# Performance work log

Hardware: AMD Instinct MI355X
Metric: run time of the kernel (lower is better)

The kernel has to match this reference:

```python
import jax, jax.numpy as jnp
import numpy as np

DIM = 3456      # visual_dim
E = 1024        # embed_dim = dim_head*heads = 128*8
H = 8
D = E // H
LN_EPS = 1e-5


def _mlp(x, w1, b1, w2, b2):
    # nn.Sequential(Linear, GELU(exact), Linear)
    h = jax.nn.gelu(x @ w1.T + b1, approximate=False)
    return h @ w2.T + b2


def _ln(x, g, b):
    m = jnp.mean(x, axis=-1, keepdims=True)
    v = jnp.mean((x - m) ** 2, axis=-1, keepdims=True)
    return (x - m) * jax.lax.rsqrt(v + LN_EPS) * g + b


def setup_inputs() -> dict:
    key = jax.random.key(0)
    ks = jax.random.split(key, 24)
    std = 0.02
    d = {"x": jax.random.normal(ks[0], (5, 729, DIM), dtype=jnp.float32)}
    i = 1
    for name in ("q", "k", "v"):
        d[f"{name}_w1"] = std * jax.random.normal(ks[i], (E, DIM), dtype=jnp.float32); i += 1
        d[f"{name}_b1"] = jnp.zeros((E,), jnp.float32)
        d[f"{name}_w2"] = std * jax.random.normal(ks[i], (E, E), dtype=jnp.float32); i += 1
        d[f"{name}_b2"] = jnp.zeros((E,), jnp.float32)
        d[f"ln_{name}_g"] = jnp.ones((E,), jnp.float32)
        d[f"ln_{name}_b"] = jnp.zeros((E,), jnp.float32)
    d["in_proj_w"] = std * jax.random.normal(ks[i], (3 * E, E), dtype=jnp.float32); i += 1
    d["in_proj_b"] = jnp.zeros((3 * E,), jnp.float32)
    d["out_proj_w"] = std * jax.random.normal(ks[i], (E, E), dtype=jnp.float32); i += 1
    d["out_proj_b"] = jnp.zeros((E,), jnp.float32)
    d["to_out_w"] = std * jax.random.normal(ks[i], (DIM, E), dtype=jnp.float32)
    return d


def reference(x,
              q_w1, q_b1, q_w2, q_b2, ln_q_g, ln_q_b,
              k_w1, k_b1, k_w2, k_b2, ln_k_g, ln_k_b,
              v_w1, v_b1, v_w2, v_b2, ln_v_g, ln_v_b,
              in_proj_w, in_proj_b, out_proj_w, out_proj_b, to_out_w):
    t, hw, c = x.shape
    # spatial_temporal pattern: x_multi = x, no interpolation.
    # q/k/v: MLP -> LN -> permute(1,0,2) -> divide_feature -> flatten.
    # divide_feature is a pure permutation of tokens; all tokens end up in a
    # single (L, 1, E) attention, so full attention over the flattened
    # (hw, t) token order computes the identical result.
    q = _ln(_mlp(x, q_w1, q_b1, q_w2, q_b2), ln_q_g, ln_q_b)  # (t, hw, E)
    k = _ln(_mlp(x, k_w1, k_b1, k_w2, k_b2), ln_k_g, ln_k_b)
    v = _ln(_mlp(x, v_w1, v_b1, v_w2, v_b2), ln_v_g, ln_v_b)
    L = t * hw
    q = q.transpose(1, 0, 2).reshape(L, E)  # (hw*t, E), (h,w,t)-major order
    k = k.transpose(1, 0, 2).reshape(L, E)
    v = v.transpose(1, 0, 2).reshape(L, E)
    # nn.MultiheadAttention with packed in_proj
    qp = (q @ in_proj_w[:E].T + in_proj_b[:E]).reshape(L, H, D)
    kp = (k @ in_proj_w[E:2 * E].T + in_proj_b[E:2 * E]).reshape(L, H, D)
    vp = (v @ in_proj_w[2 * E:].T + in_proj_b[2 * E:]).reshape(L, H, D)
    scale = 1.0 / jnp.sqrt(jnp.asarray(D, q.dtype))
    scores = jnp.einsum('qhd,khd->hqk', qp, kp) * scale  # (H, L, L)
    attn = jax.nn.softmax(scores, axis=-1)
    o = jnp.einsum('hqk,khd->qhd', attn, vp).reshape(L, E)
    o = o @ out_proj_w.T + out_proj_b
    o = o.reshape(hw, t, E).transpose(1, 0, 2)  # (t, hw, E)
    out = o @ to_out_w.T                         # (t, hw, c)
    return x + out
```

## Files before the change

### kernel.cpp

```cpp
#include <hip/hip_runtime.h>
#include <hip/hip_bf16.h>

#define L_TOK 3645
#define MP    3712
#define DIMV  3456
#define EDIM  1024

typedef __attribute__((ext_vector_type(8))) short bf8;
typedef __attribute__((ext_vector_type(4))) short s4v;
typedef __attribute__((ext_vector_type(4))) float f4;

__device__ __forceinline__ short f2b(float f) {
  union { float f; unsigned u; } v; v.f = f;
  unsigned r = v.u + 0x7fffu + ((v.u >> 16) & 1u);
  return (short)(r >> 16);
}
__device__ __forceinline__ float b2f(short s) {
  union { unsigned u; float f; } v; v.u = ((unsigned)(unsigned short)s) << 16;
  return v.f;
}
__device__ __forceinline__ void gld16(const void* g, void* l) {
  __builtin_amdgcn_global_load_lds(
      (const __attribute__((address_space(1))) void*)(unsigned long long)g,
      (__attribute__((address_space(3))) void*)(unsigned)(unsigned long long)l,
      16, 0, 0);
}

__global__ __launch_bounds__(256) void k_cvt(const float* __restrict__ src,
                                             short* __restrict__ dst, int n4) {
  int i = blockIdx.x * 256 + threadIdx.x;
  if (i >= n4) return;
  float4 v = ((const float4*)src)[i];
  s4v o; o[0] = f2b(v.x); o[1] = f2b(v.y); o[2] = f2b(v.z); o[3] = f2b(v.w);
  ((s4v*)dst)[i] = o;
}
__global__ __launch_bounds__(256) void k_cvt_pad(const float* __restrict__ src,
                                                 short* __restrict__ dst, int n4src, int n4tot) {
  int i = blockIdx.x * 256 + threadIdx.x;
  if (i >= n4tot) return;
  s4v o; o[0] = 0; o[1] = 0; o[2] = 0; o[3] = 0;
  if (i < n4src) {
    float4 v = ((const float4*)src)[i];
    o[0] = f2b(v.x); o[1] = f2b(v.y); o[2] = f2b(v.z); o[3] = f2b(v.w);
  }
  ((s4v*)dst)[i] = o;
}

#define GM_GELU   0
#define GM_BIAS   1
#define GM_QSCALE 2
#define GM_RESID  3

template<int MODE>
__global__ __launch_bounds__(256)
void k_gemm(const short* __restrict__ A, long sA,
            const short* __restrict__ B, long sB,
            const float* __restrict__ bias0, const float* __restrict__ bias1,
            const float* __restrict__ bias2,
            void* __restrict__ Cout, long sC,
            int N, int K, const float* __restrict__ resid)
{
  __shared__ short As[128 * 32];
  __shared__ short Bs[128 * 32];
  const int tid  = threadIdx.x;
  const int z    = blockIdx.z;
  const int brow = blockIdx.y * 128;
  const int bcol = blockIdx.x * 128;
  const short* Ab = A + (long)z * sA;
  const short* Bb = B + (long)z * sB;
  const float* bias = (z == 0) ? bias0 : (z == 1 ? bias1 : bias2);

  const int wave = tid >> 6, lane = tid & 63;
  const int lg = lane >> 4, lc = lane & 15;
  const int m0 = (wave >> 1) * 64, n0 = (wave & 1) * 64;

  const int r0 = tid >> 2, seg = tid & 3;
  const int r1 = r0 + 64;
  const int so0 = (seg ^ ((r0 >> 1) & 3)) * 8;
  const int so1 = (seg ^ ((r1 >> 1) & 3)) * 8;
  const short* gA0 = Ab + (long)(brow + r0) * K + so0;
  const short* gA1 = Ab + (long)(brow + r1) * K + so1;
  const short* gB0 = Bb + (long)(bcol + r0) * K + so0;
  const short* gB1 = Bb + (long)(bcol + r1) * K + so1;
  short* lA0 = &As[tid * 8];
  short* lA1 = &As[(tid + 256) * 8];
  short* lB0 = &Bs[tid * 8];
  short* lB1 = &Bs[(tid + 256) * 8];

  f4 acc[4][4];
  f4 zero = {0.f, 0.f, 0.f, 0.f};
#pragma unroll
  for (int i = 0; i < 4; ++i)
#pragma unroll
    for (int j = 0; j < 4; ++j) acc[i][j] = zero;

  for (int kt = 0; kt < K; kt += 32) {
    gld16(gA0, lA0); gld16(gA1, lA1);
    gld16(gB0, lB0); gld16(gB1, lB1);
    gA0 += 32; gA1 += 32; gB0 += 32; gB1 += 32;
    __syncthreads();
    bf8 af[4], bfr[4];
#pragma unroll
    for (int mi = 0; mi < 4; ++mi) {
      int r = m0 + mi * 16 + lc;
      af[mi] = *(const bf8*)&As[r * 32 + ((lg ^ ((r >> 1) & 3)) * 8)];
    }
#pragma unroll
    for (int ni = 0; ni < 4; ++ni) {
      int r = n0 + ni * 16 + lc;
      bfr[ni] = *(const bf8*)&Bs[r * 32 + ((lg ^ ((r >> 1) & 3)) * 8)];
    }
#pragma unroll
    for (int mi = 0; mi < 4; ++mi)
#pragma unroll
      for (int ni = 0; ni < 4; ++ni)
        acc[mi][ni] = __builtin_amdgcn_mfma_f32_16x16x32_bf16(af[mi], bfr[ni], acc[mi][ni], 0, 0, 0);
    __syncthreads();
  }

  if (MODE == GM_RESID) {
    float* C = (float*)Cout;
#pragma unroll
    for (int ni = 0; ni < 4; ++ni) {
      int col = bcol + n0 + ni * 16 + lc;
#pragma unroll
      for (int mi = 0; mi < 4; ++mi)
#pragma unroll
        for (int r = 0; r < 4; ++r) {
          int row = brow + m0 + mi * 16 + lg * 4 + r;
          if (row < L_TOK)
            C[(long)row * N + col] = acc[mi][ni][r] + resid[(long)row * N + col];
        }
    }
  } else {
    short* C = (short*)Cout + (long)z * sC;
    const float alpha = (MODE == GM_QSCALE && z == 0) ? 0.08838834764831845f : 1.0f;
#pragma unroll
    for (int ni = 0; ni < 4; ++ni) {
      int col = bcol + n0 + ni * 16 + lc;
      float bv = bias[col];
#pragma unroll
      for (int mi = 0; mi < 4; ++mi)
#pragma unroll
        for (int r = 0; r < 4; ++r) {
          int row = brow + m0 + mi * 16 + lg * 4 + r;
          float v = acc[mi][ni][r] + bv;
          if (MODE == GM_GELU) v = 0.5f * v * (1.f + erff(v * 0.70710678118654752f));
          v *= alpha;
          C[(long)row * EDIM + col] = f2b(v);
        }
    }
  }
}

__global__ __launch_bounds__(256)
void k_ln(const short* __restrict__ A, short* __restrict__ Y,
          const float* __restrict__ g0, const float* __restrict__ g1, const float* __restrict__ g2,
          const float* __restrict__ b0, const float* __restrict__ b1, const float* __restrict__ b2)
{
  const int row = blockIdx.x, z = blockIdx.y;
  const float* g = (z == 0) ? g0 : (z == 1 ? g1 : g2);
  const float* b = (z == 0) ? b0 : (z == 1 ? b1 : b2);
  const short* a = A + ((long)z * MP + row) * EDIM;
  short* y = Y + ((long)z * MP + row) * EDIM;
  const int t = threadIdx.x;
  s4v v = *(const s4v*)&a[t * 4];
  float x0 = b2f(v[0]), x1 = b2f(v[1]), x2 = b2f(v[2]), x3 = b2f(v[3]);
  float s = x0 + x1 + x2 + x3;
  float q = x0 * x0 + x1 * x1 + x2 * x2 + x3 * x3;
#pragma unroll
  for (int off = 1; off < 64; off <<= 1) { s += __shfl_xor(s, off); q += __shfl_xor(q, off); }
  __shared__ float rs[4], rq[4];
  if ((t & 63) == 0) { rs[t >> 6] = s; rq[t >> 6] = q; }
  __syncthreads();
  s = rs[0] + rs[1] + rs[2] + rs[3];
  q = rq[0] + rq[1] + rq[2] + rq[3];
  float mean = s * (1.f / 1024.f);
  float var  = q * (1.f / 1024.f) - mean * mean;
  float rstd = rsqrtf(var + 1e-5f);
  s4v o;
#pragma unroll
  for (int j = 0; j < 4; ++j) {
    int col = t * 4 + j;
    o[j] = f2b((b2f(v[j]) - mean) * rstd * g[col] + b[col]);
  }
  *(s4v*)&y[t * 4] = o;
}

__global__ __launch_bounds__(256)
void k_vtrans(const short* __restrict__ vp, short* __restrict__ vpT)
{
  const int kb = blockIdx.x * 64, h = blockIdx.y;
  __shared__ short T[64 * 128];
  const int tid = threadIdx.x;
#pragma unroll
  for (int i = 0; i < 4; ++i) {
    int c = tid + 256 * i;
    int r = c >> 4, x = c & 15;
    bf8 val = *(const bf8*)&vp[(long)(kb + r) * EDIM + h * 128 + x * 8];
    *(bf8*)&T[r * 128 + ((x ^ (r & 7)) * 8)] = val;
  }
  __syncthreads();
#pragma unroll
  for (int i = 0; i < 4; ++i) {
    int c = tid + 256 * i;
    int dr = c >> 3, x = c & 7;
    short tmp[8];
#pragma unroll
    for (int e = 0; e < 8; ++e) {
      int kv = x * 8 + e;
      tmp[e] = T[kv * 128 + (((dr >> 3) ^ (kv & 7)) << 3) + (dr & 7)];
    }
    *(bf8*)&vpT[((long)h * 128 + dr) * MP + kb + x * 8] = *(bf8*)tmp;
  }
}

__global__ __launch_bounds__(256)
void k_attn(const short* __restrict__ qp, const short* __restrict__ kp,
            const short* __restrict__ vpT, short* __restrict__ o)
{
  const int bx = blockIdx.x;
  const int h = bx & 7, qb = (bx >> 3) * 64;
  const int tid = threadIdx.x, wave = tid >> 6, lane = tid & 63;
  const int lg = lane >> 4, lc = lane & 15;
  __shared__ short Ks[64 * 128];
  __shared__ short Vs[128 * 64];
  __shared__ short Ps[4][16 * 64];

  const int qrow = qb + wave * 16 + lc;
  bf8 qf[4];
#pragma unroll
  for (int d4 = 0; d4 < 4; ++d4)
    qf[d4] = *(const bf8*)&qp[(long)qrow * EDIM + h * 128 + d4 * 32 + lg * 8];

  f4 oacc[8];
  f4 zero = {0.f, 0.f, 0.f, 0.f};
#pragma unroll
  for (int dt = 0; dt < 8; ++dt) oacc[dt] = zero;
  float lsum = 0.f;

  for (int kb = 0; kb < L_TOK; kb += 64) {
#pragma unroll
    for (int i = 0; i < 4; ++i) {
      int c = tid + 256 * i; int r = c >> 4, x = c & 15;
      gld16(&kp[(long)(kb + r) * EDIM + h * 128 + (x ^ (r & 7)) * 8], &Ks[c * 8]);
    }
#pragma unroll
    for (int i = 0; i < 4; ++i) {
      int c = tid + 256 * i; int dr = c >> 3, x = c & 7;
      gld16(&vpT[((long)h * 128 + dr) * MP + kb + (x ^ (dr & 7)) * 8], &Vs[c * 8]);
    }
    __syncthreads();

#pragma unroll
    for (int s = 0; s < 4; ++s) {
      f4 sa = zero;
      const int krow = s * 16 + lc;
#pragma unroll
      for (int d4 = 0; d4 < 4; ++d4) {
        bf8 kf = *(const bf8*)&Ks[krow * 128 + (((d4 * 4 + lg) ^ (krow & 7)) * 8)];
        sa = __builtin_amdgcn_mfma_f32_16x16x32_bf16(kf, qf[d4], sa, 0, 0, 0);
      }
      const int kvb = kb + s * 16 + lg * 4;
      float p[4];
#pragma unroll
      for (int r = 0; r < 4; ++r) {
        float e = __expf(sa[r]);
        p[r] = (kvb + r < L_TOK) ? e : 0.f;
        lsum += p[r];
      }
      s4v pk; pk[0] = f2b(p[0]); pk[1] = f2b(p[1]); pk[2] = f2b(p[2]); pk[3] = f2b(p[3]);
      *(s4v*)&Ps[wave][lc * 64 + ((s * 16 + lg * 4) ^ ((lc & 7) << 3))] = pk;
    }
    bf8 pf0 = *(const bf8*)&Ps[wave][lc * 64 + ((lg * 8) ^ ((lc & 7) << 3))];
    bf8 pf1 = *(const bf8*)&Ps[wave][lc * 64 + ((32 + lg * 8) ^ ((lc & 7) << 3))];
#pragma unroll
    for (int dt = 0; dt < 8; ++dt) {
      const int vrow = dt * 16 + lc;
      bf8 vf0 = *(const bf8*)&Vs[vrow * 64 + ((lg ^ (vrow & 7)) * 8)];
      bf8 vf1 = *(const bf8*)&Vs[vrow * 64 + (((4 + lg) ^ (vrow & 7)) * 8)];
      oacc[dt] = __builtin_amdgcn_mfma_f32_16x16x32_bf16(pf0, vf0, oacc[dt], 0, 0, 0);
      oacc[dt] = __builtin_amdgcn_mfma_f32_16x16x32_bf16(pf1, vf1, oacc[dt], 0, 0, 0);
    }
    __syncthreads();
  }

  lsum += __shfl_xor(lsum, 16);
  lsum += __shfl_xor(lsum, 32);
  float rinv[4];
#pragma unroll
  for (int r = 0; r < 4; ++r) rinv[r] = 1.f / __shfl(lsum, lg * 4 + r);
#pragma unroll
  for (int dt = 0; dt < 8; ++dt)
#pragma unroll
    for (int r = 0; r < 4; ++r) {
      int orow = qb + wave * 16 + lg * 4 + r;
      o[(long)orow * EDIM + h * 128 + dt * 16 + lc] = f2b(oacc[dt][r] * rinv[r]);
    }
}

extern "C" void kernel_launch(void* const* d_in, const int* in_sizes, int n_in,
                              void* d_out, int out_size, void* d_ws, size_t ws_size,
                              hipStream_t stream)
{
  const float* x   = (const float*)d_in[0];
  const float* ipb = (const float*)d_in[20];
  const float* opb = (const float*)d_in[22];

  char* ws = (char*)d_ws;
  short* regA = (short*)(ws + 0);
  short* regB = (short*)(ws + 25657344);
  short* w1b  = (short*)(ws + 48463872);
  short* w2b  = (short*)(ws + 69697536);
  short* wpb  = (short*)(ws + 75988992);
  short* wob  = (short*)(ws + 82280448);
  short* wtb  = (short*)(ws + 84377600);
  short* vpT  = (short*)(ws + 91455488);

  short* xb  = regA;
  short* h1  = regB;
  short* aln = regA;
  short* lnq = regB;
  short* proj = regA;
  short* ob  = regB;
  short* o2  = (short*)(ws + 25657344 + 7602176);

  k_cvt_pad<<<12528, 256, 0, stream>>>(x, xb, 3149280, 3207168);
  k_cvt<<<3456, 256, 0, stream>>>((const float*)d_in[1],  w1b,            884736);
  k_cvt<<<3456, 256, 0, stream>>>((const float*)d_in[7],  w1b + 3538944,  884736);
  k_cvt<<<3456, 256, 0, stream>>>((const float*)d_in[13], w1b + 7077888,  884736);
  k_cvt<<<1024, 256, 0, stream>>>((const float*)d_in[3],  w2b,            262144);
  k_cvt<<<1024, 256, 0, stream>>>((const float*)d_in[9],  w2b + 1048576,  262144);
  k_cvt<<<1024, 256, 0, stream>>>((const float*)d_in[15], w2b + 2097152,  262144);
  k_cvt<<<3072, 256, 0, stream>>>((const float*)d_in[19], wpb,            786432);
  k_cvt<<<1024, 256, 0, stream>>>((const float*)d_in[21], wob,            262144);
  k_cvt<<<3456, 256, 0, stream>>>((const float*)d_in[23], wtb,            884736);

  dim3 g3(8, 29, 3), g1(8, 29, 1);
  k_gemm<GM_GELU><<<g3, 256, 0, stream>>>(xb, 0, w1b, 3538944,
      (const float*)d_in[2], (const float*)d_in[8], (const float*)d_in[14],
      h1, (long)MP * EDIM, EDIM, DIMV, nullptr);
  k_gemm<GM_BIAS><<<g3, 256, 0, stream>>>(h1, (long)MP * EDIM, w2b, 1048576,
      (const float*)d_in[4], (const float*)d_in[10], (const float*)d_in[16],
      aln, (long)MP * EDIM, EDIM, EDIM, nullptr);
  dim3 gl(MP, 3);
  k_ln<<<gl, 256, 0, stream>>>(aln, lnq,
      (const float*)d_in[5], (const float*)d_in[11], (const float*)d_in[17],
      (const float*)d_in[6], (const float*)d_in[12], (const float*)d_in[18]);
  k_gemm<GM_QSCALE><<<g3, 256, 0, stream>>>(lnq, (long)MP * EDIM, wpb, 1048576,
      ipb, ipb + 1024, ipb + 2048,
      proj, (long)MP * EDIM, EDIM, EDIM, nullptr);
  dim3 gt(MP / 64, 8);
  k_vtrans<<<gt, 256, 0, stream>>>(proj + 2L * MP * EDIM, vpT);
  k_attn<<<(MP / 64) * 8, 256, 0, stream>>>(proj, proj + (long)MP * EDIM, vpT, ob);
  k_gemm<GM_BIAS><<<g1, 256, 0, stream>>>(ob, 0, wob, 0,
      opb, opb, opb, o2, 0, EDIM, EDIM, nullptr);
  dim3 g5(27, 29, 1);
  k_gemm<GM_RESID><<<g5, 256, 0, stream>>>(o2, 0, wtb, 0,
      nullptr, nullptr, nullptr, d_out, 0, DIMV, EDIM, x);
}
```

Measured before the change: 486.3 us.

## Triple-buffer GEMM LDS loads and swizzle workgroups across XCDs

The GEMM main loop now uses three LDS buffers with global_load_lds prefetch two tiles ahead, using vmcnt waits and a single barrier per iteration instead of two syncthreads. This is meant to hide global memory latency behind MFMA work. Workgroup IDs are also remapped so that consecutive tiles land on the same XCD, which should improve L2 reuse. The cost is three times the LDS per block, which may lower occupancy.

Measured after the change: 444.7 us. -8.6%, faster.

```diff
diff --git a/kernel.cpp b/kernel.cpp
--- a/kernel.cpp
+++ b/kernel.cpp
@@ -60,12 +60,19 @@
             void* __restrict__ Cout, long sC,
             int N, int K, const float* __restrict__ resid)
 {
-  __shared__ short As[128 * 32];
-  __shared__ short Bs[128 * 32];
+  __shared__ short As[3][128 * 32];
+  __shared__ short Bs[3][128 * 32];
   const int tid  = threadIdx.x;
   const int z    = blockIdx.z;
-  const int brow = blockIdx.y * 128;
-  const int bcol = blockIdx.x * 128;
+
+  const int nwg  = gridDim.x * gridDim.y;
+  const int orig = blockIdx.y * gridDim.x + blockIdx.x;
+  const int qq   = nwg >> 3, rr = nwg & 7;
+  const int xcd  = orig & 7, ofs = orig >> 3;
+  const int swz  = (xcd < rr ? xcd * (qq + 1) : rr * (qq + 1) + (xcd - rr) * qq) + ofs;
+  const int brow = (swz / gridDim.x) * 128;
+  const int bcol = (swz % gridDim.x) * 128;
+
   const short* Ab = A + (long)z * sA;
   const short* Bb = B + (long)z * sB;
   const float* bias = (z == 0) ? bias0 : (z == 1 ? bias1 : bias2);
@@ -78,14 +85,10 @@
   const int r1 = r0 + 64;
   const int so0 = (seg ^ ((r0 >> 1) & 3)) * 8;
   const int so1 = (seg ^ ((r1 >> 1) & 3)) * 8;
-  const short* gA0 = Ab + (long)(brow + r0) * K + so0;
-  const short* gA1 = Ab + (long)(brow + r1) * K + so1;
-  const short* gB0 = Bb + (long)(bcol + r0) * K + so0;
-  const short* gB1 = Bb + (long)(bcol + r1) * K + so1;
-  short* lA0 = &As[tid * 8];
-  short* lA1 = &As[(tid + 256) * 8];
-  short* lB0 = &Bs[tid * 8];
-  short* lB1 = &Bs[(tid + 256) * 8];
+  const short* pA0 = Ab + (long)(brow + r0) * K + so0;
+  const short* pA1 = Ab + (long)(brow + r1) * K + so1;
+  const short* pB0 = Bb + (long)(bcol + r0) * K + so0;
+  const short* pB1 = Bb + (long)(bcol + r1) * K + so1;
 
   f4 acc[4][4];
   f4 zero = {0.f, 0.f, 0.f, 0.f};
@@ -94,28 +97,45 @@
 #pragma unroll
     for (int j = 0; j < 4; ++j) acc[i][j] = zero;
 
-  for (int kt = 0; kt < K; kt += 32) {
-    gld16(gA0, lA0); gld16(gA1, lA1);
-    gld16(gB0, lB0); gld16(gB1, lB1);
-    gA0 += 32; gA1 += 32; gB0 += 32; gB1 += 32;
-    __syncthreads();
+  auto STAGE = [&](int buf) {
+    gld16(pA0, &As[buf][tid * 8]);
+    gld16(pA1, &As[buf][(tid + 256) * 8]);
+    gld16(pB0, &Bs[buf][tid * 8]);
+    gld16(pB1, &Bs[buf][(tid + 256) * 8]);
+    pA0 += 32; pA1 += 32; pB0 += 32; pB1 += 32;
+  };
+
+  const int NT = K >> 5;
+  STAGE(0);
+  STAGE(1);
+
+  for (int t = 0; t < NT; ++t) {
+    const int buf = t % 3;
+    if (t < NT - 1) { asm volatile("s_waitcnt vmcnt(4)" ::: "memory"); }
+    else           { asm volatile("s_waitcnt vmcnt(0)" ::: "memory"); }
+    __builtin_amdgcn_sched_barrier(0);
+    __builtin_amdgcn_s_barrier();
+    if (t + 2 < NT) STAGE((t + 2) % 3);
+
+    const short* Al = &As[buf][0];
+    const short* Bl = &Bs[buf][0];
     bf8 af[4], bfr[4];
 #pragma unroll
     for (int mi = 0; mi < 4; ++mi) {
       int r = m0 + mi * 16 + lc;
-      af[mi] = *(const bf8*)&As[r * 32 + ((lg ^ ((r >> 1) & 3)) * 8)];
+      af[mi] = *(const bf8*)&Al[r * 32 + ((lg ^ ((r >> 1) & 3)) * 8)];
     }
 #pragma unroll
     for (int ni = 0; ni < 4; ++ni) {
       int r = n0 + ni * 16 + lc;
-      bfr[ni] = *(const bf8*)&Bs[r * 32 + ((lg ^ ((r >> 1) & 3)) * 8)];
+      bfr[ni] = *(const bf8*)&Bl[r * 32 + ((lg ^ ((r >> 1) & 3)) * 8)];
     }
 #pragma unroll
     for (int mi = 0; mi < 4; ++mi)
 #pragma unroll
       for (int ni = 0; ni < 4; ++ni)
         acc[mi][ni] = __builtin_amdgcn_mfma_f32_16x16x32_bf16(af[mi], bfr[ni], acc[mi][ni], 0, 0, 0);
-    __syncthreads();
+    __builtin_amdgcn_sched_barrier(0);
   }
 
   if (MODE == GM_RESID) {
```
